# Kernel tuning notes

Measured on AMD Instinct MI355X. Metric: run time of the kernel, lower is better.

The kernel has to match this reference:

```python
import jax, jax.numpy as jnp
import numpy as np

NEGPOS_RATIO = 3


def _smooth_l1(pred, tgt):
    d = jnp.abs(pred - tgt)
    return jnp.where(d < 1.0, 0.5 * d * d, d - 0.5)


def setup_inputs() -> dict:
    key = jax.random.key(0)
    B, P, C = 64, 8732, 81
    ks = jax.random.split(key, 7)
    loc_dataT = jax.random.normal(ks[0], (B, P, 4), jnp.float32)
    conf_dataT = jax.random.normal(ks[1], (B, P, C), jnp.float32)
    loc_dataS = jax.random.normal(ks[2], (B, P, 4), jnp.float32)
    conf_dataS = jax.random.normal(ks[3], (B, P, C), jnp.float32)
    loc_t = jax.random.normal(ks[4], (B, P, 4), jnp.float32)
    is_pos = jax.random.uniform(ks[5], (B, P)) < 0.02
    labels = jax.random.randint(ks[6], (B, P), 1, C, dtype=jnp.int32)
    conf_t = jnp.where(is_pos, labels, 0).astype(jnp.int32)
    return {
        "loc_dataT": loc_dataT, "conf_dataT": conf_dataT,
        "loc_dataS": loc_dataS, "conf_dataS": conf_dataS,
        "loc_t": loc_t, "conf_t": conf_t,
    }


def _multibox_losses(loc_dataT, conf_dataT, loc_dataS, conf_dataS, loc_t, conf_t):
    B, P, C = conf_dataT.shape
    pos = conf_t > 0                                    # [B,P]
    posf = pos.astype(conf_dataT.dtype)

    # Localization SmoothL1 over positive priors (reduction='sum')
    loss_lT = jnp.sum(_smooth_l1(loc_dataT, loc_t) * posf[..., None])
    loss_lS = jnp.sum(_smooth_l1(loc_dataS, loc_t) * posf[..., None])

    # Per-prior CE loss: logsumexp(conf) - conf[gt]  (== -log_softmax[gt])
    def per_prior_ce(conf):
        lse = jax.nn.logsumexp(conf, axis=-1)           # [B,P]
        gt = jnp.take_along_axis(conf, conf_t[..., None].astype(jnp.int32), axis=-1)[..., 0]
        return lse - gt

    lcT = per_prior_ce(conf_dataT)                      # [B,P]
    lcS = per_prior_ce(conf_dataS)

    # Hard negative mining: rank negatives by loss (positives zeroed first)
    def neg_mask(lc, num_neg):
        lc_m = jnp.where(pos, 0.0, lc)
        order = jnp.argsort(-lc_m, axis=1)              # descending sort indices
        rank = jnp.argsort(order, axis=1)               # rank of each prior
        return rank < num_neg

    num_pos = jnp.sum(pos.astype(jnp.int32), axis=1, keepdims=True)   # [B,1]
    num_neg = jnp.minimum(NEGPOS_RATIO * num_pos, P - 1)
    negT = neg_mask(lcT, num_neg)
    negS = neg_mask(lcS, num_neg)

    # Confidence CE over positives + mined negatives (reduction='sum')
    loss_cT = jnp.sum(jnp.where(pos | negT, lcT, 0.0))
    loss_cS = jnp.sum(jnp.where(pos | negS, lcS, 0.0))

    N = jnp.sum(num_pos).astype(conf_dataT.dtype)
    return jnp.stack([loss_lT / N, loss_cT / N, loss_lS / N, loss_cS / N])


def reference(loc_dataT, conf_dataT, loc_dataS, conf_dataS, loc_t, conf_t):
    # Teacher branch is detached in the original module.
    loc_dataT = jax.lax.stop_gradient(loc_dataT)
    conf_dataT = jax.lax.stop_gradient(conf_dataT)
    return _multibox_losses(loc_dataT, conf_dataT, loc_dataS, conf_dataS, loc_t, conf_t)
```

## Files before the change

### kernel.cpp

```cpp
#include <hip/hip_runtime.h>
#include <hip/hip_bf16.h>

#define BB 64
#define PP 8732
#define CC 81
#define RPB 128
#define SLOTS ((RPB * CC) / 4)


__device__ __forceinline__ float sl1(float d) {
    d = fabsf(d);
    return d < 1.0f ? 0.5f * d * d : d - 0.5f;
}

__device__ __forceinline__ float blockReduceF(float v, volatile float* sb) {
    for (int off = 32; off; off >>= 1) v += __shfl_xor(v, off, 64);
    __syncthreads();
    if ((threadIdx.x & 63) == 0) sb[threadIdx.x >> 6] = v;
    __syncthreads();
    float r = 0.0f;
    int nw = blockDim.x >> 6;
    for (int i = 0; i < nw; ++i) r += sb[i];
    return r;
}

__device__ __forceinline__ int blockReduceI(int v, volatile int* sb) {
    for (int off = 32; off; off >>= 1) v += __shfl_xor(v, off, 64);
    __syncthreads();
    if ((threadIdx.x & 63) == 0) sb[threadIdx.x >> 6] = v;
    __syncthreads();
    int r = 0;
    int nw = blockDim.x >> 6;
    for (int i = 0; i < nw; ++i) r += sb[i];
    return r;
}

__global__ void kInit(float* acc, int* numpos) {
    int t = threadIdx.x;
    if (t < 4) acc[t] = 0.0f;
    if (t < BB) numpos[t] = 0;
}

__global__ __launch_bounds__(1024) void kA(const float4* __restrict__ locT,
                                           const float4* __restrict__ locS,
                                           const float4* __restrict__ loct,
                                           const int* __restrict__ conft,
                                           float* acc, int* numpos) {
    __shared__ float fsb[16];
    __shared__ int isb[16];
    int b = blockIdx.y;
    int p = blockIdx.x * blockDim.x + threadIdx.x;
    float sT = 0.0f, sS = 0.0f;
    int cnt = 0;
    if (p < PP) {
        size_t i = (size_t)b * PP + p;
        int t = conft[i];
        if (t > 0) {
            cnt = 1;
            float4 g = loct[i];
            float4 aT = locT[i];
            float4 aS = locS[i];
            sT = sl1(aT.x - g.x) + sl1(aT.y - g.y) + sl1(aT.z - g.z) + sl1(aT.w - g.w);
            sS = sl1(aS.x - g.x) + sl1(aS.y - g.y) + sl1(aS.z - g.z) + sl1(aS.w - g.w);
        }
    }
    sT = blockReduceF(sT, fsb);
    sS = blockReduceF(sS, fsb);
    cnt = blockReduceI(cnt, isb);
    if (threadIdx.x == 0) {
        if (sT != 0.0f) atomicAdd(&acc[0], sT);
        if (sS != 0.0f) atomicAdd(&acc[1], sS);
        if (cnt) atomicAdd(&numpos[b], cnt);
    }
}

__device__ __forceinline__ void processSlot(int i, float4 v,
                                            float* psum, float* spill) {
    int f = i << 2;
    int r0 = f / 81;
    int rem = f - r0 * 81;
    float e0 = __expf(v.x), e1 = __expf(v.y), e2 = __expf(v.z), e3 = __expf(v.w);
    float t01 = e0 + e1;
    float tot = t01 + e2 + e3;
    float ps = tot;
    if (rem >= 78) {
        int ns = 81 - rem;
        float a = (ns == 1) ? e0 : ((ns == 2) ? t01 : t01 + e2);
        ps = a;
        spill[r0 + 1] = tot - a;
    }
    psum[i] = ps;
}

__global__ __launch_bounds__(256, 6) void kB(const float* __restrict__ confT,
                                             const float* __restrict__ confS,
                                             const int* __restrict__ conft,
                                             float* __restrict__ lcT,
                                             float* __restrict__ lcS) {
    __shared__ float psum[SLOTS];
    __shared__ float spill[RPB];
    __shared__ float gtval[RPB];
    __shared__ int gtraw[RPB];
    int b = blockIdx.y;
    int p0 = blockIdx.x * RPB;
    int nrows = min(RPB, PP - p0);
    int tid = threadIdx.x;
    const float* __restrict__ conf = blockIdx.z ? confS : confT;
    float* __restrict__ dst = blockIdx.z ? lcS : lcT;
    size_t rowBase = (size_t)b * PP + p0;
    const float* __restrict__ rowp = conf + rowBase * CC;
    const float4* __restrict__ g4 = (const float4*)rowp;

    if (nrows == RPB) {
        int g_ = 0;
        if (tid < RPB) g_ = conft[rowBase + tid];
        float4 v[10];
        #pragma unroll
        for (int k = 0; k < 10; ++k) v[k] = g4[tid + 256 * k];
        float4 vx;
        bool extra = tid < (SLOTS - 2560);
        if (extra) vx = g4[2560 + tid];
        float gtv = 0.0f;
        if (tid < RPB) gtv = rowp[tid * CC + g_];
        __builtin_amdgcn_sched_barrier(0);
        #pragma unroll
        for (int k = 0; k < 10; ++k)
            processSlot(tid + 256 * k, v[k], psum, spill);
        if (extra) processSlot(2560 + tid, vx, psum, spill);
        if (tid < RPB) { gtraw[tid] = g_; gtval[tid] = gtv; }
    } else {
        int nq = (nrows * CC) >> 2;
        int g_ = 0;
        if (tid < nrows) g_ = conft[rowBase + tid];
        for (int i = tid; i < nq; i += 256)
            processSlot(i, g4[i], psum, spill);
        if (tid < nrows) { gtraw[tid] = g_; gtval[tid] = rowp[tid * CC + g_]; }
    }
    __syncthreads();

    int r = tid >> 1, h = tid & 1;
    if (r < nrows) {
        int i0 = (81 * r + 3) >> 2;
        int i1 = (81 * (r + 1) + 3) >> 2;
        int mid = (i0 + i1 + 1) >> 1;
        int lo = h ? mid : i0;
        int hi = h ? i1 : mid;
        float s = (h == 0 && (r & 3)) ? spill[r] : 0.0f;
        for (int i = lo; i < hi; ++i) s += psum[i];
        s += __shfl_xor(s, 1, 64);
        if (h == 0) {
            float lc = __logf(s) - gtval[r];
            dst[rowBase + r] = (gtraw[r] > 0) ? -(lc + 1.0f) : lc;
        }
    }
}

__global__ __launch_bounds__(1024) void kC(const float* __restrict__ lcT,
                                           const float* __restrict__ lcS,
                                           const int* __restrict__ numpos,
                                           float* acc) {
    __shared__ unsigned keys[PP];
    __shared__ int hist[256];
    __shared__ float fsb[16];
    __shared__ int isb[16];
    __shared__ int selBin, selAbove;
    int b = blockIdx.y;
    int tid = threadIdx.x;
    const float* src = ((blockIdx.x == 0) ? lcT : lcS) + (size_t)b * PP;

    float posSum = 0.0f;
    for (int i = tid; i < PP; i += 1024) {
        float v = src[i];
        keys[i] = (v < 0.0f) ? 0u : __float_as_uint(v);
        if (v < 0.0f) posSum += (-v - 1.0f);
    }
    posSum = blockReduceF(posSum, fsb);

    int np = numpos[b];
    int k = min(3 * np, PP - 1);
    float mined = 0.0f;
    if (k > 0) {
        unsigned prefix = 0;
        int kk = k;
        for (int round = 0; round < 4; ++round) {
            int shift = 24 - 8 * round;
            if (tid < 256) hist[tid] = 0;
            __syncthreads();
            for (int i = tid; i < PP; i += 1024) {
                unsigned key = keys[i];
                bool match = (round == 0) || ((key >> (shift + 8)) == prefix);
                if (match) atomicAdd(&hist[(key >> shift) & 0xFF], 1);
            }
            __syncthreads();
            for (int d = 1; d < 256; d <<= 1) {
                int v2 = 0;
                if (tid < 256) v2 = hist[tid] + ((tid + d < 256) ? hist[tid + d] : 0);
                __syncthreads();
                if (tid < 256) hist[tid] = v2;
                __syncthreads();
            }
            if (tid < 256) {
                int above = (tid < 255) ? hist[tid + 1] : 0;
                if (above < kk && hist[tid] >= kk) {
                    selBin = tid;
                    selAbove = above;
                }
            }
            __syncthreads();
            prefix = (prefix << 8) | (unsigned)selBin;
            kk -= selAbove;
            __syncthreads();
        }
        int c = 0;
        float s = 0.0f;
        for (int i = tid; i < PP; i += 1024) {
            unsigned key = keys[i];
            if (key > prefix) { c += 1; s += __uint_as_float(key); }
        }
        c = blockReduceI(c, isb);
        s = blockReduceF(s, fsb);
        mined = s + (float)(k - c) * __uint_as_float(prefix);
    }
    if (tid == 0) atomicAdd(&acc[(blockIdx.x == 0) ? 2 : 3], posSum + mined);
}

__global__ void kD(const float* acc, const int* numpos, float* out) {
    int v = (threadIdx.x < BB) ? numpos[threadIdx.x] : 0;
    for (int off = 32; off; off >>= 1) v += __shfl_xor(v, off, 64);
    if (threadIdx.x == 0) {
        float N = (float)v;
        out[0] = acc[0] / N;
        out[1] = acc[2] / N;
        out[2] = acc[1] / N;
        out[3] = acc[3] / N;
    }
}

extern "C" void kernel_launch(void* const* d_in, const int* in_sizes, int n_in,
                              void* d_out, int out_size, void* d_ws, size_t ws_size,
                              hipStream_t stream) {
    const float* locT  = (const float*)d_in[0];
    const float* confT = (const float*)d_in[1];
    const float* locS  = (const float*)d_in[2];
    const float* confS = (const float*)d_in[3];
    const float* loct  = (const float*)d_in[4];
    const int*   conft = (const int*)d_in[5];
    float* out = (float*)d_out;

    float* lcT = (float*)d_ws;
    float* lcS = lcT + (size_t)BB * PP;
    float* acc = lcS + (size_t)BB * PP;
    int* numpos = (int*)(acc + 4);

    kInit<<<1, 64, 0, stream>>>(acc, numpos);

    dim3 gA((PP + 1023) / 1024, BB);
    kA<<<gA, 1024, 0, stream>>>((const float4*)locT, (const float4*)locS,
                                (const float4*)loct, conft, acc, numpos);

    dim3 gB((PP + RPB - 1) / RPB, BB, 2);
    kB<<<gB, 256, 0, stream>>>(confT, confS, conft, lcT, lcS);

    dim3 gC(2, BB);
    kC<<<gC, 1024, 0, stream>>>(lcT, lcS, numpos, acc);

    kD<<<1, 64, 0, stream>>>(acc, numpos, out);
}
```

Measured before the change: 423.3 us.

## Fuse loc loss into CE kernel, per-wave histograms, fold finalize into last block

Merges the localization kernel into the per-prior CE kernel. Each 512-thread block now processes both teacher and student confidence rows for 128 priors, and the student loads are issued while the teacher rows are being reduced. The radix-select histogram is privatized per wave to cut LDS atomic contention. The final normalization kernel is replaced by a last-block-done counter inside the mining kernel. Together these remove two launches and add overlap, at the cost of higher register and LDS pressure and a threadfence/atomic protocol.

```diff
diff --git a/kernel.cpp b/kernel.cpp
--- a/kernel.cpp
+++ b/kernel.cpp
@@ -1,11 +1,11 @@
 #include <hip/hip_runtime.h>
-#include <hip/hip_bf16.h>
 
 #define BB 64
 #define PP 8732
 #define CC 81
 #define RPB 128
 #define SLOTS ((RPB * CC) / 4)
+#define TPB 512
 
 
 __device__ __forceinline__ float sl1(float d) {
@@ -35,43 +35,11 @@
     return r;
 }
 
-__global__ void kInit(float* acc, int* numpos) {
+__global__ void kInit(float* acc, int* numpos, int* ctr) {
     int t = threadIdx.x;
     if (t < 4) acc[t] = 0.0f;
     if (t < BB) numpos[t] = 0;
-}
-
-__global__ __launch_bounds__(1024) void kA(const float4* __restrict__ locT,
-                                           const float4* __restrict__ locS,
-                                           const float4* __restrict__ loct,
-                                           const int* __restrict__ conft,
-                                           float* acc, int* numpos) {
-    __shared__ float fsb[16];
-    __shared__ int isb[16];
-    int b = blockIdx.y;
-    int p = blockIdx.x * blockDim.x + threadIdx.x;
-    float sT = 0.0f, sS = 0.0f;
-    int cnt = 0;
-    if (p < PP) {
-        size_t i = (size_t)b * PP + p;
-        int t = conft[i];
-        if (t > 0) {
-            cnt = 1;
-            float4 g = loct[i];
-            float4 aT = locT[i];
-            float4 aS = locS[i];
-            sT = sl1(aT.x - g.x) + sl1(aT.y - g.y) + sl1(aT.z - g.z) + sl1(aT.w - g.w);
-            sS = sl1(aS.x - g.x) + sl1(aS.y - g.y) + sl1(aS.z - g.z) + sl1(aS.w - g.w);
-        }
-    }
-    sT = blockReduceF(sT, fsb);
-    sS = blockReduceF(sS, fsb);
-    cnt = blockReduceI(cnt, isb);
-    if (threadIdx.x == 0) {
-        if (sT != 0.0f) atomicAdd(&acc[0], sT);
-        if (sS != 0.0f) atomicAdd(&acc[1], sS);
-        if (cnt) atomicAdd(&numpos[b], cnt);
-    }
+    if (t == 0) ctr[0] = 0;
 }
 
 __device__ __forceinline__ void processSlot(int i, float4 v,
@@ -92,52 +60,10 @@
     psum[i] = ps;
 }
 
-__global__ __launch_bounds__(256, 6) void kB(const float* __restrict__ confT,
-                                             const float* __restrict__ confS,
-                                             const int* __restrict__ conft,
-                                             float* __restrict__ lcT,
-                                             float* __restrict__ lcS) {
-    __shared__ float psum[SLOTS];
-    __shared__ float spill[RPB];
-    __shared__ float gtval[RPB];
-    __shared__ int gtraw[RPB];
-    int b = blockIdx.y;
-    int p0 = blockIdx.x * RPB;
-    int nrows = min(RPB, PP - p0);
-    int tid = threadIdx.x;
-    const float* __restrict__ conf = blockIdx.z ? confS : confT;
-    float* __restrict__ dst = blockIdx.z ? lcS : lcT;
-    size_t rowBase = (size_t)b * PP + p0;
-    const float* __restrict__ rowp = conf + rowBase * CC;
-    const float4* __restrict__ g4 = (const float4*)rowp;
-
-    if (nrows == RPB) {
-        int g_ = 0;
-        if (tid < RPB) g_ = conft[rowBase + tid];
-        float4 v[10];
-        #pragma unroll
-        for (int k = 0; k < 10; ++k) v[k] = g4[tid + 256 * k];
-        float4 vx;
-        bool extra = tid < (SLOTS - 2560);
-        if (extra) vx = g4[2560 + tid];
-        float gtv = 0.0f;
-        if (tid < RPB) gtv = rowp[tid * CC + g_];
-        __builtin_amdgcn_sched_barrier(0);
-        #pragma unroll
-        for (int k = 0; k < 10; ++k)
-            processSlot(tid + 256 * k, v[k], psum, spill);
-        if (extra) processSlot(2560 + tid, vx, psum, spill);
-        if (tid < RPB) { gtraw[tid] = g_; gtval[tid] = gtv; }
-    } else {
-        int nq = (nrows * CC) >> 2;
-        int g_ = 0;
-        if (tid < nrows) g_ = conft[rowBase + tid];
-        for (int i = tid; i < nq; i += 256)
-            processSlot(i, g4[i], psum, spill);
-        if (tid < nrows) { gtraw[tid] = g_; gtval[tid] = rowp[tid * CC + g_]; }
-    }
-    __syncthreads();
-
+__device__ __forceinline__ void phase2(float* __restrict__ dst, size_t rowBase,
+                                       int nrows, int tid,
+                                       const float* psum, const float* spill,
+                                       const float* gtval, const int* gtraw) {
     int r = tid >> 1, h = tid & 1;
     if (r < nrows) {
         int i0 = (81 * r + 3) >> 2;
@@ -155,15 +81,124 @@
     }
 }
 
+__global__ __launch_bounds__(TPB, 6) void kMain(
+        const float* __restrict__ confT, const float* __restrict__ confS,
+        const int* __restrict__ conft,
+        const float4* __restrict__ locT4, const float4* __restrict__ locS4,
+        const float4* __restrict__ loct4,
+        float* __restrict__ lcT, float* __restrict__ lcS,
+        float* acc, int* numpos) {
+    __shared__ float psum[SLOTS];
+    __shared__ float spill[RPB];
+    __shared__ float gtval[RPB];
+    __shared__ int gtraw[RPB];
+    __shared__ float fsb[TPB / 64];
+    __shared__ int isb[TPB / 64];
+
+    int b = blockIdx.y;
+    int p0 = blockIdx.x * RPB;
+    int nrows = min(RPB, PP - p0);
+    int tid = threadIdx.x;
+    size_t rowBase = (size_t)b * PP + p0;
+    const float* __restrict__ rowT = confT + rowBase * CC;
+    const float* __restrict__ rowS = confS + rowBase * CC;
+    const float4* __restrict__ gT = (const float4*)rowT;
+    const float4* __restrict__ gS = (const float4*)rowS;
+
+    bool hasrow = tid < nrows;
+    int g_ = 0;
+    if (hasrow) g_ = conft[rowBase + tid];
+
+    float sT = 0.0f, sS = 0.0f;
+    int cnt = 0;
+
+    if (nrows == RPB) {
+        float4 v[5];
+        #pragma unroll
+        for (int k = 0; k < 5; ++k) v[k] = gT[tid + TPB * k];
+        float4 vx;
+        bool extra = tid < (SLOTS - 5 * TPB);
+        if (extra) vx = gT[5 * TPB + tid];
+        float gtvT = 0.0f, gtvS = 0.0f;
+        if (hasrow) {
+            gtvT = rowT[tid * CC + g_];
+            gtvS = rowS[tid * CC + g_];
+            if (g_ > 0) {
+                size_t idx = rowBase + tid;
+                float4 gt = loct4[idx];
+                float4 aT = locT4[idx];
+                float4 aS = locS4[idx];
+                sT = sl1(aT.x - gt.x) + sl1(aT.y - gt.y) + sl1(aT.z - gt.z) + sl1(aT.w - gt.w);
+                sS = sl1(aS.x - gt.x) + sl1(aS.y - gt.y) + sl1(aS.z - gt.z) + sl1(aS.w - gt.w);
+                cnt = 1;
+            }
+        }
+        #pragma unroll
+        for (int k = 0; k < 5; ++k) processSlot(tid + TPB * k, v[k], psum, spill);
+        if (extra) processSlot(5 * TPB + tid, vx, psum, spill);
+        float4 w[5];
+        #pragma unroll
+        for (int k = 0; k < 5; ++k) w[k] = gS[tid + TPB * k];
+        float4 wx;
+        if (extra) wx = gS[5 * TPB + tid];
+        if (hasrow) { gtraw[tid] = g_; gtval[tid] = gtvT; }
+        __syncthreads();
+        phase2(lcT, rowBase, nrows, tid, psum, spill, gtval, gtraw);
+        __syncthreads();
+        #pragma unroll
+        for (int k = 0; k < 5; ++k) processSlot(tid + TPB * k, w[k], psum, spill);
+        if (extra) processSlot(5 * TPB + tid, wx, psum, spill);
+        if (hasrow) gtval[tid] = gtvS;
+        __syncthreads();
+        phase2(lcS, rowBase, nrows, tid, psum, spill, gtval, gtraw);
+    } else {
+        int nq = (nrows * CC) >> 2;
+        float gtvT = 0.0f, gtvS = 0.0f;
+        if (hasrow) {
+            gtvT = rowT[tid * CC + g_];
+            gtvS = rowS[tid * CC + g_];
+            if (g_ > 0) {
+                size_t idx = rowBase + tid;
+                float4 gt = loct4[idx];
+                float4 aT = locT4[idx];
+                float4 aS = locS4[idx];
+                sT = sl1(aT.x - gt.x) + sl1(aT.y - gt.y) + sl1(aT.z - gt.z) + sl1(aT.w - gt.w);
+                sS = sl1(aS.x - gt.x) + sl1(aS.y - gt.y) + sl1(aS.z - gt.z) + sl1(aS.w - gt.w);
+                cnt = 1;
+            }
+        }
+        for (int i = tid; i < nq; i += TPB) processSlot(i, gT[i], psum, spill);
+        if (hasrow) { gtraw[tid] = g_; gtval[tid] = gtvT; }
+        __syncthreads();
+        phase2(lcT, rowBase, nrows, tid, psum, spill, gtval, gtraw);
+        __syncthreads();
+        for (int i = tid; i < nq; i += TPB) processSlot(i, gS[i], psum, spill);
+        if (hasrow) gtval[tid] = gtvS;
+        __syncthreads();
+        phase2(lcS, rowBase, nrows, tid, psum, spill, gtval, gtraw);
+    }
+
+    sT = blockReduceF(sT, fsb);
+    sS = blockReduceF(sS, fsb);
+    cnt = blockReduceI(cnt, isb);
+    if (tid == 0) {
+        if (sT != 0.0f) atomicAdd(&acc[0], sT);
+        if (sS != 0.0f) atomicAdd(&acc[1], sS);
+        if (cnt) atomicAdd(&numpos[b], cnt);
+    }
+}
+
 __global__ __launch_bounds__(1024) void kC(const float* __restrict__ lcT,
                                            const float* __restrict__ lcS,
                                            const int* __restrict__ numpos,
-                                           float* acc) {
+                                           float* acc, int* ctr,
+                                           float* __restrict__ out) {
     __shared__ unsigned keys[PP];
+    __shared__ int whist[16 * 256];
     __shared__ int hist[256];
     __shared__ float fsb[16];
     __shared__ int isb[16];
-    __shared__ int selBin, selAbove;
+    __shared__ int selBin, selAbove, lastFlag;
     int b = blockIdx.y;
     int tid = threadIdx.x;
     const float* src = ((blockIdx.x == 0) ? lcT : lcS) + (size_t)b * PP;
@@ -182,14 +217,22 @@
     if (k > 0) {
         unsigned prefix = 0;
         int kk = k;
+        int wid = tid >> 6;
         for (int round = 0; round < 4; ++round) {
             int shift = 24 - 8 * round;
-            if (tid < 256) hist[tid] = 0;
+            for (int i = tid; i < 16 * 256; i += 1024) whist[i] = 0;
             __syncthreads();
             for (int i = tid; i < PP; i += 1024) {
                 unsigned key = keys[i];
                 bool match = (round == 0) || ((key >> (shift + 8)) == prefix);
-                if (match) atomicAdd(&hist[(key >> shift) & 0xFF], 1);
+                if (match) atomicAdd(&whist[(wid << 8) | ((key >> shift) & 0xFF)], 1);
+            }
+            __syncthreads();
+            if (tid < 256) {
+                int h2 = 0;
+                #pragma unroll
+                for (int w = 0; w < 16; ++w) h2 += whist[(w << 8) | tid];
+                hist[tid] = h2;
             }
             __syncthreads();
             for (int d = 1; d < 256; d <<= 1) {
@@ -221,18 +264,31 @@
         s = blockReduceF(s, fsb);
         mined = s + (float)(k - c) * __uint_as_float(prefix);
     }
-    if (tid == 0) atomicAdd(&acc[(blockIdx.x == 0) ? 2 : 3], posSum + mined);
-}
-
-__global__ void kD(const float* acc, const int* numpos, float* out) {
-    int v = (threadIdx.x < BB) ? numpos[threadIdx.x] : 0;
-    for (int off = 32; off; off >>= 1) v += __shfl_xor(v, off, 64);
-    if (threadIdx.x == 0) {
-        float N = (float)v;
-        out[0] = acc[0] / N;
-        out[1] = acc[2] / N;
-        out[2] = acc[1] / N;
-        out[3] = acc[3] / N;
+    if (tid == 0) {
+        atomicAdd(&acc[(blockIdx.x == 0) ? 2 : 3], posSum + mined);
+        __threadfence();
+        int old = atomicAdd(ctr, 1);
+        lastFlag = (old == 2 * BB - 1) ? 1 : 0;
+    }
+    __syncthreads();
+    if (lastFlag) {
+        __threadfence();
+        int v = 0;
+        if (tid < BB)
+            v = __hip_atomic_load(&numpos[tid], __ATOMIC_RELAXED, __HIP_MEMORY_SCOPE_AGENT);
+        if (tid < 64)
+            for (int off = 32; off; off >>= 1) v += __shfl_xor(v, off, 64);
+        if (tid == 0) {
+            float N = (float)v;
+            float a0 = __hip_atomic_load(&acc[0], __ATOMIC_RELAXED, __HIP_MEMORY_SCOPE_AGENT);
+            float a1 = __hip_atomic_load(&acc[1], __ATOMIC_RELAXED, __HIP_MEMORY_SCOPE_AGENT);
+            float a2 = __hip_atomic_load(&acc[2], __ATOMIC_RELAXED, __HIP_MEMORY_SCOPE_AGENT);
+            float a3 = __hip_atomic_load(&acc[3], __ATOMIC_RELAXED, __HIP_MEMORY_SCOPE_AGENT);
+            out[0] = a0 / N;
+            out[1] = a2 / N;
+            out[2] = a1 / N;
+            out[3] = a3 / N;
+        }
     }
 }
 
@@ -251,18 +307,15 @@
     float* lcS = lcT + (size_t)BB * PP;
     float* acc = lcS + (size_t)BB * PP;
     int* numpos = (int*)(acc + 4);
-
-    kInit<<<1, 64, 0, stream>>>(acc, numpos);
-
-    dim3 gA((PP + 1023) / 1024, BB);
-    kA<<<gA, 1024, 0, stream>>>((const float4*)locT, (const float4*)locS,
-                                (const float4*)loct, conft, acc, numpos);
-
-    dim3 gB((PP + RPB - 1) / RPB, BB, 2);
-    kB<<<gB, 256, 0, stream>>>(confT, confS, conft, lcT, lcS);
+    int* ctr = numpos + BB;
+
+    kInit<<<1, 64, 0, stream>>>(acc, numpos, ctr);
+
+    dim3 gM((PP + RPB - 1) / RPB, BB);
+    kMain<<<gM, TPB, 0, stream>>>(confT, confS, conft,
+                                  (const float4*)locT, (const float4*)locS,
+                                  (const float4*)loct, lcT, lcS, acc, numpos);
 
     dim3 gC(2, BB);
-    kC<<<gC, 1024, 0, stream>>>(lcT, lcS, numpos, acc);
-
-    kD<<<1, 64, 0, stream>>>(acc, numpos, out);
-}
+    kC<<<gC, 1024, 0, stream>>>(lcT, lcS, numpos, acc, ctr, out);
+}
```

Measured after the change: 440.4 us. 4.0% more time.
